# Kernel tuning notes

Measured on AMD Instinct MI355X. Metric: run time of the kernel, lower is better.

The kernel has to match this reference:

```python
import jax, jax.numpy as jnp
import numpy as np

NUM_GROUPS = 32
EPS = 1e-6


def group_norm(x, gamma, beta):
    # x: [b, c, h, w]
    b, c, h, w = x.shape
    g = NUM_GROUPS
    xg = x.reshape(b, g, c // g, h, w)
    mean = xg.mean(axis=(2, 3, 4), keepdims=True)
    var = xg.var(axis=(2, 3, 4), keepdims=True)
    xn = ((xg - mean) * jax.lax.rsqrt(var + EPS)).reshape(b, c, h, w)
    return xn * gamma[None, :, None, None] + beta[None, :, None, None]


def conv1x1(x, w, b):
    # x: [b, c, h, w], w: [out_c, in_c], b: [out_c]
    return jnp.einsum('bchw,oc->bohw', x, w) + b[None, :, None, None]


def setup_inputs() -> dict:
    key = jax.random.key(0)
    ks = jax.random.split(key, 11)
    B, C, H, W = 4, 512, 64, 64
    s = 1.0 / np.sqrt(C)
    inp = {
        'x': jax.random.normal(ks[0], (B, C, H, W), dtype=jnp.float32),
        'gn_gamma': jnp.ones((C,), dtype=jnp.float32),
        'gn_beta': jnp.zeros((C,), dtype=jnp.float32),
        'wq': jax.random.normal(ks[1], (C, C), dtype=jnp.float32) * s,
        'bq': jax.random.normal(ks[2], (C,), dtype=jnp.float32) * 0.01,
        'wk': jax.random.normal(ks[3], (C, C), dtype=jnp.float32) * s,
        'bk': jax.random.normal(ks[4], (C,), dtype=jnp.float32) * 0.01,
        'wv': jax.random.normal(ks[5], (C, C), dtype=jnp.float32) * s,
        'bv': jax.random.normal(ks[6], (C,), dtype=jnp.float32) * 0.01,
        'wo': jax.random.normal(ks[7], (C, C), dtype=jnp.float32) * s,
        'bo': jax.random.normal(ks[8], (C,), dtype=jnp.float32) * 0.01,
    }
    return inp


def reference(x, gn_gamma, gn_beta, wq, bq, wk, bk, wv, bv, wo, bo):
    b, c, h, w = x.shape
    h_ = group_norm(x, gn_gamma, gn_beta)
    q = conv1x1(h_, wq, bq).reshape(b, c, h * w)  # [b, c, n]
    k = conv1x1(h_, wk, bk).reshape(b, c, h * w)
    v = conv1x1(h_, wv, bv).reshape(b, c, h * w)
    scale = jnp.asarray(c, x.dtype) ** -0.5
    # attn[b, i, j] = softmax_j(q_i . k_j * scale)
    attn = jax.nn.softmax(jnp.einsum('bci,bcj->bij', q, k) * scale, axis=-1)
    # A[b, c, i] = sum_j attn[b, i, j] * v[b, c, j]
    A = jnp.einsum('bij,bcj->bci', attn, v).reshape(b, c, h, w)
    A = conv1x1(A, wo, bo)
    # NOTE: the original module multiplies (not adds) the input by the attention output
    return x * A
```

## Files before the change

kernel.cpp:

```cpp
#include <hip/hip_runtime.h>
#include <hip/hip_bf16.h>
#include <stdint.h>

typedef __bf16 bf16x8 __attribute__((ext_vector_type(8)));
typedef __bf16 bf16x4 __attribute__((ext_vector_type(4)));
typedef float f32x4 __attribute__((ext_vector_type(4)));

__device__ __forceinline__ void gload_lds16(const __bf16* g, __bf16* l) {
  __builtin_amdgcn_global_load_lds(
      (const __attribute__((address_space(1))) void*)g,
      (__attribute__((address_space(3))) void*)l, 16, 0, 0);
}

__global__ __launch_bounds__(256) void cvt4_kernel(const float* __restrict__ s0,
                                                   const float* __restrict__ s1,
                                                   const float* __restrict__ s2,
                                                   const float* __restrict__ s3,
                                                   __bf16* __restrict__ dst) {
  int i = blockIdx.x * 256 + threadIdx.x;
  const float* srcs[4] = {s0, s1, s2, s3};
  int m = i >> 18;
  dst[i] = (__bf16)srcs[m][i & 262143];
}

__global__ __launch_bounds__(256) void biascat_kernel(const float* __restrict__ bq,
                                                      const float* __restrict__ bk,
                                                      float* __restrict__ bqk) {
  int i = blockIdx.x * 256 + threadIdx.x;
  bqk[i] = (i < 512) ? bq[i] : bk[i - 512];
}

__global__ __launch_bounds__(256) void gn1a_kernel(const float* __restrict__ x,
                                                   __bf16* __restrict__ xbf,
                                                   float2* __restrict__ part) {
  const int tid = threadIdx.x;
  const size_t base4 = ((size_t)blockIdx.x * 8192) >> 2;
  const float4* x4 = (const float4*)x;
  bf16x4* o4 = (bf16x4*)xbf;

  float s1 = 0.f, s2 = 0.f;
#pragma unroll
  for (int j = 0; j < 8; ++j) {
    float4 t = x4[base4 + tid + j * 256];
    s1 += t.x + t.y + t.z + t.w;
    s2 += t.x * t.x + t.y * t.y + t.z * t.z + t.w * t.w;
    bf16x4 o;
    o[0] = (__bf16)t.x; o[1] = (__bf16)t.y; o[2] = (__bf16)t.z; o[3] = (__bf16)t.w;
    o4[base4 + tid + j * 256] = o;
  }
#pragma unroll
  for (int off = 32; off; off >>= 1) {
    s1 += __shfl_xor(s1, off);
    s2 += __shfl_xor(s2, off);
  }
  __shared__ float r1[4], r2[4];
  if ((tid & 63) == 0) { r1[tid >> 6] = s1; r2[tid >> 6] = s2; }
  __syncthreads();
  if (tid == 0)
    part[blockIdx.x] = float2{r1[0] + r1[1] + r1[2] + r1[3],
                              r2[0] + r2[1] + r2[2] + r2[3]};
}

__global__ __launch_bounds__(512) void gn1b_kernel(const float2* __restrict__ part,
                                                   const float* __restrict__ gamma,
                                                   const float* __restrict__ beta,
                                                   float2* __restrict__ gmbt) {
  const int b = blockIdx.x;
  const int t = threadIdx.x;
  __shared__ float sm[32], si[32];
  if (t < 32) {
    float s1 = 0.f, s2 = 0.f;
#pragma unroll
    for (int j = 0; j < 8; ++j) {
      float2 p = part[(b * 32 + t) * 8 + j];
      s1 += p.x; s2 += p.y;
    }
    const float mean = s1 * (1.f / 65536.f);
    const float var = s2 * (1.f / 65536.f) - mean * mean;
    sm[t] = mean;
    si[t] = rsqrtf(var + 1e-6f);
  }
  __syncthreads();
  const int g = t >> 4;
  const float gm = gamma[t] * si[g];
  gmbt[b * 512 + t] = float2{gm, beta[t] - sm[g] * gm};
}

__global__ __launch_bounds__(256) void gn2_kernel(const __bf16* __restrict__ xbf,
                                                  const float2* __restrict__ gmbt,
                                                  __bf16* __restrict__ hnT) {
  const int b = blockIdx.z;
  const int c0 = blockIdx.y * 64;
  const int n0 = blockIdx.x * 64;
  const int t = threadIdx.x;
  __shared__ __bf16 tile[64][72];

  {
    const int row = t >> 2;
    const int col = (t & 3) * 16;
    const __bf16* src = xbf + ((size_t)(b * 512 + c0 + row)) * 4096 + n0 + col;
    bf16x8 u0 = *(const bf16x8*)src;
    bf16x8 u1 = *(const bf16x8*)(src + 8);
    *(bf16x8*)&tile[row][col] = u0;
    *(bf16x8*)&tile[row][col + 8] = u1;
  }
  __syncthreads();
  {
    const int nrow = t >> 2;
    const int cc = (t & 3) * 16;
    bf16x8 o0, o1;
#pragma unroll
    for (int j = 0; j < 16; ++j) {
      const int c = c0 + cc + j;
      float2 s = gmbt[b * 512 + c];
      float val = (float)tile[cc + j][nrow] * s.x + s.y;
      if (j < 8) o0[j] = (__bf16)val; else o1[j - 8] = (__bf16)val;
    }
    __bf16* dst = hnT + ((size_t)b * 4096 + n0 + nrow) * 512 + c0 + cc;
    *(bf16x8*)dst = o0;
    *(bf16x8*)(dst + 8) = o1;
  }
}

__global__ __launch_bounds__(256) void rowsum_inv_kernel(const __bf16* __restrict__ P,
                                                         float* __restrict__ inv) {
  const int r = blockIdx.x * 4 + (threadIdx.x >> 6);
  const int lane = threadIdx.x & 63;
  const bf16x8* rp = (const bf16x8*)(P + (size_t)r * 4096);
  float s = 0.f;
#pragma unroll
  for (int j = 0; j < 8; ++j) {
    bf16x8 v = rp[lane + j * 64];
#pragma unroll
    for (int e = 0; e < 8; ++e) s += (float)v[e];
  }
#pragma unroll
  for (int off = 32; off; off >>= 1) s += __shfl_xor(s, off);
  if (lane == 0) inv[r] = 1.0f / s;
}

template <int BIAS, int EEXP, int RSCALE, int KC>
__global__ __launch_bounds__(256) void gemm4w_kernel(
    const __bf16* __restrict__ A, int lda, long long sA,
    const __bf16* __restrict__ Bm, int ldb, long long sB,
    __bf16* __restrict__ Out, int ldo, long long sO,
    const float* __restrict__ bias, const float* __restrict__ rowinv,
    float scale) {
  constexpr int SLOT = 4096;
  constexpr int BST = 72;
  __shared__ __bf16 sm[8 * SLOT];
  __bf16* smB = sm + 4 * SLOT;

  const int gx = gridDim.x, gxy = gx * gridDim.y;
  const int nwg = gxy * gridDim.z;
  int bid = blockIdx.x + gx * blockIdx.y + gxy * blockIdx.z;
  bid = (bid & 7) * (nwg >> 3) + (bid >> 3);
  const int bz = bid / gxy;
  const int rem = bid - bz * gxy;
  const int by = rem / gx, bx = rem - by * gx;
  const int tm0 = by * 128, tn0 = bx * 128;

  const int t = threadIdx.x;
  const int lane = t & 63, wid = t >> 6;
  const int wr = wid >> 1, wc = wid & 1;

  const __bf16* Az = A + (size_t)bz * sA;
  const __bf16* Bz = Bm + (size_t)bz * sB;

  const int scol = ((t & 3) * 8) ^ (((t >> 3) & 3) * 8);
  const __bf16* gA0 = Az + (size_t)(tm0 + (t >> 2)) * lda + scol;
  const __bf16* gA1 = gA0 + (size_t)64 * lda;
  const __bf16* gB0 = Bz + (size_t)(tn0 + (t >> 2)) * ldb + scol;
  const __bf16* gB1 = gB0 + (size_t)64 * ldb;
  __bf16* dA = sm + t * 8;
  __bf16* dB = smB + t * 8;

  auto stage = [&](int ks) {
    const int sl = ks & 3;
    gload_lds16(gA0 + (size_t)ks * 32, dA + sl * SLOT);
    gload_lds16(gA1 + (size_t)ks * 32, dA + sl * SLOT + 2048);
    gload_lds16(gB0 + (size_t)ks * 32, dB + sl * SLOT);
    gload_lds16(gB1 + (size_t)ks * 32, dB + sl * SLOT + 2048);
  };

  const int lr = lane & 15;
  const int kb = ((lane >> 4) * 16) ^ ((lr & 6) << 3);
  const __bf16* rdA = sm + (((wr * 64 + lr) * 64 + kb) >> 1);
  const __bf16* rdB = smB + (((wc * 64 + lr) * 64 + kb) >> 1);

  f32x4 acc[4][4];
#pragma unroll
  for (int i = 0; i < 4; ++i)
#pragma unroll
    for (int j = 0; j < 4; ++j) acc[i][j] = f32x4{0.f, 0.f, 0.f, 0.f};
  bf16x8 av[4], bv[4];

  auto rdfr = [&](int sl) {
#pragma unroll
    for (int m = 0; m < 4; ++m) av[m] = *(const bf16x8*)(rdA + sl * SLOT + m * 512);
#pragma unroll
    for (int n = 0; n < 4; ++n) bv[n] = *(const bf16x8*)(rdB + sl * SLOT + n * 512);
  };
  auto mma16 = [&] {
    __builtin_amdgcn_s_barrier();
    __builtin_amdgcn_s_setprio(1);
#pragma unroll
    for (int m = 0; m < 4; ++m)
#pragma unroll
      for (int n = 0; n < 4; ++n)
        acc[m][n] = __builtin_amdgcn_mfma_f32_16x16x32_bf16(av[m], bv[n], acc[m][n], 0, 0, 0);
    __builtin_amdgcn_s_setprio(0);
  };

  constexpr int TOT = KC / 32;

  stage(0); stage(1); stage(2);
  asm volatile("s_waitcnt vmcnt(8)" ::: "memory");
  __builtin_amdgcn_s_barrier();

#pragma unroll 1
  for (int s = 0; s < TOT - 3; ++s) {
    rdfr(s & 3);
    stage(s + 3);
    mma16();
    asm volatile("s_waitcnt vmcnt(8)" ::: "memory");
    __builtin_amdgcn_s_barrier();
  }
  rdfr((TOT - 3) & 3); mma16();
  asm volatile("s_waitcnt vmcnt(4)" ::: "memory");
  __builtin_amdgcn_s_barrier();
  rdfr((TOT - 2) & 3); mma16();
  asm volatile("s_waitcnt vmcnt(0)" ::: "memory");
  __builtin_amdgcn_s_barrier();
  rdfr((TOT - 1) & 3); mma16();
  __builtin_amdgcn_s_barrier();

  __bf16* bnc = sm + wid * 16 * BST;
  const int q4 = (lane >> 4) * 4;
  const int row0 = tm0 + wr * 64;
  const int wn = tn0 + wc * 64;
  float bcol[4];
#pragma unroll
  for (int n = 0; n < 4; ++n) bcol[n] = BIAS ? bias[wn + n * 16 + lr] : 0.f;
#pragma unroll
  for (int m = 0; m < 4; ++m) {
    float ri[4];
    if constexpr (RSCALE) {
#pragma unroll
      for (int r = 0; r < 4; ++r)
        ri[r] = rowinv[(size_t)bz * 4096 + row0 + m * 16 + q4 + r];
    }
#pragma unroll
    for (int n = 0; n < 4; ++n)
#pragma unroll
      for (int r = 0; r < 4; ++r) {
        float val = acc[m][n][r] * scale + bcol[n];
        if constexpr (EEXP) val = exp2f(val * 1.44269504f);
        if constexpr (RSCALE) val *= ri[r];
        bnc[(q4 + r) * BST + n * 16 + lr] = (__bf16)val;
      }
    const int rr = lane >> 3, c8 = (lane & 7) * 8;
    bf16x8 v0 = *(const bf16x8*)&bnc[rr * BST + c8];
    bf16x8 v1 = *(const bf16x8*)&bnc[(rr + 8) * BST + c8];
    __bf16* op = Out + (size_t)bz * sO +
                 (size_t)(row0 + m * 16 + rr) * ldo + wn + c8;
    *(bf16x8*)op = v0;
    *(bf16x8*)(op + (size_t)8 * ldo) = v1;
  }
}

template <int EPI, int BIAS>
__global__ __launch_bounds__(256) void gemm_lds_kernel(
    const __bf16* __restrict__ A, int lda, long long sA,
    const __bf16* __restrict__ Bm, int ldb, long long sB,
    void* __restrict__ Out, int ldo, long long sO,
    const float* __restrict__ bias, const __bf16* __restrict__ xmul,
    long long sX, float scale, int K) {
  __shared__ __bf16 sTa[2][128 * 32];
  __shared__ __bf16 sTb[2][128 * 32];

  const int gx = gridDim.x, gxy = gx * gridDim.y;
  const int nwg = gxy * gridDim.z;
  int bid = blockIdx.x + gx * blockIdx.y + gxy * blockIdx.z;
  if ((nwg & 7) == 0) bid = (bid & 7) * (nwg >> 3) + (bid >> 3);
  const int bz = bid / gxy;
  const int rem = bid - bz * gxy;
  const int by = rem / gx;
  const int bx = rem - by * gx;

  const int tid = threadIdx.x;
  const int lane = tid & 63;
  const int wid = tid >> 6;
  const int wr = wid >> 1, wc = wid & 1;
  const int tm0 = by * 128, tn0 = bx * 128;
  const int lr = lane & 15, lk = (lane >> 4) * 8;

  const int ch0 = wid * 2;
  const int srow = lane >> 2;
  const int scol = (lane & 3) * 8;
  const __bf16* gA0 = A + (size_t)bz * sA + (size_t)(tm0 + ch0 * 16 + srow) * lda + scol;
  const __bf16* gB0 = Bm + (size_t)bz * sB + (size_t)(tn0 + ch0 * 16 + srow) * ldb + scol;
  const size_t stepA = (size_t)16 * lda, stepB = (size_t)16 * ldb;

  f32x4 acc[4][4];
#pragma unroll
  for (int i = 0; i < 4; ++i)
#pragma unroll
    for (int j = 0; j < 4; ++j) acc[i][j] = f32x4{0.f, 0.f, 0.f, 0.f};

  const int T = K >> 5;
  gload_lds16(gA0, &sTa[0][ch0 * 512]);
  gload_lds16(gA0 + stepA, &sTa[0][ch0 * 512 + 512]);
  gload_lds16(gB0, &sTb[0][ch0 * 512]);
  gload_lds16(gB0 + stepB, &sTb[0][ch0 * 512 + 512]);

  for (int tt = 0; tt < T; ++tt) {
    __syncthreads();
    const int cur = tt & 1;
    if (tt + 1 < T) {
      const __bf16* a = gA0 + (size_t)(tt + 1) * 32;
      const __bf16* b = gB0 + (size_t)(tt + 1) * 32;
      gload_lds16(a, &sTa[cur ^ 1][ch0 * 512]);
      gload_lds16(a + stepA, &sTa[cur ^ 1][ch0 * 512 + 512]);
      gload_lds16(b, &sTb[cur ^ 1][ch0 * 512]);
      gload_lds16(b + stepB, &sTb[cur ^ 1][ch0 * 512 + 512]);
    }
    const __bf16* fa = &sTa[cur][(wr * 64 + lr) * 32 + lk];
    const __bf16* fb = &sTb[cur][(wc * 64 + lr) * 32 + lk];
    bf16x8 a[4], b[4];
#pragma unroll
    for (int i = 0; i < 4; ++i) a[i] = *(const bf16x8*)(fa + i * 512);
#pragma unroll
    for (int j = 0; j < 4; ++j) b[j] = *(const bf16x8*)(fb + j * 512);
#pragma unroll
    for (int i = 0; i < 4; ++i)
#pragma unroll
      for (int j = 0; j < 4; ++j)
        acc[i][j] = __builtin_amdgcn_mfma_f32_16x16x32_bf16(a[i], b[j], acc[i][j], 0, 0, 0);
  }

  const int wm = tm0 + wr * 64, wn = tn0 + wc * 64;
#pragma unroll
  for (int i = 0; i < 4; ++i) {
#pragma unroll
    for (int r = 0; r < 4; ++r) {
      const int row = wm + i * 16 + (lane >> 4) * 4 + r;
#pragma unroll
      for (int j = 0; j < 4; ++j) {
        const int col = wn + j * 16 + lr;
        float val = acc[i][j][r] * scale;
        if (BIAS == 1) val += bias[col];
        if (BIAS == 2) val += bias[row];
        const size_t off = (size_t)bz * sO + (size_t)row * ldo + col;
        if (EPI == 0) {
          ((__bf16*)Out)[off] = (__bf16)val;
        } else if (EPI == 1) {
          ((float*)Out)[off] = val;
        } else {
          ((float*)Out)[off] = (float)xmul[(size_t)bz * sX + (size_t)row * ldo + col] * val;
        }
      }
    }
  }
}

extern "C" void kernel_launch(void* const* d_in, const int* in_sizes, int n_in,
                              void* d_out, int out_size, void* d_ws, size_t ws_size,
                              hipStream_t stream) {
  const int C = 512, N = 4096;
  const float* x = (const float*)d_in[0];
  const float* gng = (const float*)d_in[1];
  const float* gnb = (const float*)d_in[2];
  const float* wq = (const float*)d_in[3];
  const float* bq = (const float*)d_in[4];
  const float* wk = (const float*)d_in[5];
  const float* bk = (const float*)d_in[6];
  const float* wv = (const float*)d_in[7];
  const float* bv = (const float*)d_in[8];
  const float* wo = (const float*)d_in[9];
  const float* bo = (const float*)d_in[10];

  char* ws = (char*)d_ws;
  const size_t MB = 1ull << 20;
  const long long NC = (long long)N * C;
  const long long NN = (long long)N * N;
  const long long NQK = (long long)N * 1024;
  const bool batched = ws_size >= 194 * MB + 32768;

  __bf16 *S, *qkT, *a2T, *v, *xbf, *wqB;
  char* misc;
  if (batched) {
    S   = (__bf16*)(ws);
    qkT = (__bf16*)(ws + 128 * MB);
    a2T = qkT;
    v   = (__bf16*)(ws + 160 * MB);
    xbf = (__bf16*)(ws + 176 * MB);
    wqB = (__bf16*)(ws + 192 * MB);
    misc = ws + 194 * MB;
  } else {
    S   = (__bf16*)(ws);
    qkT = (__bf16*)(ws + 32 * MB);
    a2T = (__bf16*)(ws + 64 * MB);
    v   = (__bf16*)(ws + 80 * MB);
    xbf = (__bf16*)(ws + 96 * MB);
    wqB = (__bf16*)(ws + 112 * MB);
    misc = ws + 114 * MB;
  }
  __bf16* hnT = (__bf16*)ws;
  __bf16* wvB = wqB + 2 * 262144;
  __bf16* woB = wvB + 262144;
  float* bqk   = (float*)misc;
  float2* gmbt = (float2*)(misc + 4096);
  float2* part = (float2*)(misc + 20480);
  float* rowInv = (float*)d_out;

  const float scl = 0.044194173824159216f;

  cvt4_kernel<<<4096, 256, 0, stream>>>(wq, wk, wv, wo, wqB);
  biascat_kernel<<<4, 256, 0, stream>>>(bq, bk, bqk);
  gn1a_kernel<<<1024, 256, 0, stream>>>(x, xbf, part);
  gn1b_kernel<<<4, 512, 0, stream>>>(part, gng, gnb, gmbt);
  gn2_kernel<<<dim3(64, 8, 4), 256, 0, stream>>>(xbf, gmbt, hnT);

  gemm4w_kernel<1, 0, 0, 512><<<dim3(8, 32, 4), 256, 0, stream>>>(
      hnT, C, NC, wqB, C, 0, qkT, 1024, NQK, bqk, nullptr, 1.f);
  gemm_lds_kernel<0, 2><<<dim3(32, 4, 4), 256, 0, stream>>>(
      wvB, C, 0, hnT, C, NC, v, N, NC, bv, nullptr, 0, 1.f, C);

  if (batched) {
    gemm4w_kernel<0, 1, 0, 512><<<dim3(32, 32, 4), 256, 0, stream>>>(
        qkT, 1024, NQK, qkT + 512, 1024, NQK, S, N, NN, nullptr, nullptr, scl);
    rowsum_inv_kernel<<<4096, 256, 0, stream>>>(S, rowInv);
    gemm4w_kernel<0, 0, 1, 4096><<<dim3(4, 32, 4), 256, 0, stream>>>(
        S, N, NN, v, N, NC, a2T, C, NC, nullptr, rowInv, 1.f);
  } else {
    for (int b = 0; b < 4; ++b) {
      gemm4w_kernel<0, 1, 0, 512><<<dim3(32, 32, 1), 256, 0, stream>>>(
          qkT + (size_t)b * NQK, 1024, 0, qkT + (size_t)b * NQK + 512, 1024, 0,
          S, N, 0, nullptr, nullptr, scl);
      rowsum_inv_kernel<<<1024, 256, 0, stream>>>(S, rowInv);
      gemm4w_kernel<0, 0, 1, 4096><<<dim3(4, 32, 1), 256, 0, stream>>>(
          S, N, 0, v + (size_t)b * NC, N, 0, a2T + (size_t)b * NC, C, 0,
          nullptr, rowInv, 1.f);
    }
  }

  gemm_lds_kernel<2, 2><<<dim3(32, 4, 4), 256, 0, stream>>>(
      woB, C, 0, a2T, C, NC, (float*)d_out, N, NC, bo, xbf, NC, 1.f, C);
}
```

Baseline: 289.1 us.

## Fuse softmax rowsum into PV GEMM, add large-tile QK exp kernel, unify GEMMs

Removes the separate rowsum kernel by computing row sums of the exponentiated scores inside the P·V GEMM, using an extra MFMA against a ones vector, and normalising in the epilogue. Adds a dedicated 512-thread QK^T+exp kernel with 1024x256 tiles that reuses each loaded K tile across four row sub-tiles. Replaces the older double-buffered gemm_lds kernel for the V projection and output projection with the 4-stage gemm4w pipeline. The trade-offs are extra MFMA work, higher register pressure in the large-tile kernel, and a much smaller grid for QK.

New measurement: 264.2 us. -8.6%, faster.

```diff
diff --git a/kernel.cpp b/kernel.cpp
--- a/kernel.cpp
+++ b/kernel.cpp
@@ -122,30 +122,145 @@
   }
 }
 
-__global__ __launch_bounds__(256) void rowsum_inv_kernel(const __bf16* __restrict__ P,
-                                                         float* __restrict__ inv) {
-  const int r = blockIdx.x * 4 + (threadIdx.x >> 6);
-  const int lane = threadIdx.x & 63;
-  const bf16x8* rp = (const bf16x8*)(P + (size_t)r * 4096);
-  float s = 0.f;
-#pragma unroll
-  for (int j = 0; j < 8; ++j) {
-    bf16x8 v = rp[lane + j * 64];
-#pragma unroll
-    for (int e = 0; e < 8; ++e) s += (float)v[e];
-  }
-#pragma unroll
-  for (int off = 32; off; off >>= 1) s += __shfl_xor(s, off);
-  if (lane == 0) inv[r] = 1.0f / s;
-}
-
-template <int BIAS, int EEXP, int RSCALE, int KC>
+__global__ __launch_bounds__(512) void qkexp_kernel(
+    const __bf16* __restrict__ q, const __bf16* __restrict__ k,
+    __bf16* __restrict__ S, long long sQ, long long sS, float scale) {
+  constexpr int BST = 72;
+  __shared__ __bf16 sm[8 * 8192 + 8 * 16 * BST];
+  __bf16* smB = sm + 4 * 8192;
+  __bf16* smE = sm + 8 * 8192;
+
+  const int gx = gridDim.x, gxy = gx * gridDim.y;
+  const int nwg = gxy * gridDim.z;
+  int bid = blockIdx.x + gx * blockIdx.y + gxy * blockIdx.z;
+  bid = (bid & 7) * (nwg >> 3) + (bid >> 3);
+  const int bz = bid / gxy;
+  const int rem = bid - bz * gxy;
+  const int by = rem / gx, bx = rem - by * gx;
+  const int tm0 = by * 1024, tn0 = bx * 256;
+
+  const int t = threadIdx.x;
+  const int lane = t & 63, wid = t >> 6;
+  const int wr = wid >> 2, wc = wid & 3;
+
+  const int scol = ((t & 3) * 8) ^ (((t >> 3) & 3) * 8);
+  const __bf16* gA0 = q + (size_t)bz * sQ + (size_t)(tm0 + (t >> 2)) * 1024 + scol;
+  const __bf16* gA1 = gA0 + (size_t)128 * 1024;
+  const __bf16* gB0 = k + (size_t)bz * sQ + (size_t)(tn0 + (t >> 2)) * 1024 + scol;
+  const __bf16* gB1 = gB0 + (size_t)128 * 1024;
+  __bf16* dA = sm + t * 8;
+  __bf16* dB = smB + t * 8;
+
+  auto stageA = [&](int sig) {
+    const int st_ = sig >> 4, ks = sig & 15, sl = sig & 3;
+    const size_t off = (size_t)(st_ * 256) * 1024 + ks * 32;
+    gload_lds16(gA0 + off, dA + sl * 8192);
+    gload_lds16(gA1 + off, dA + sl * 8192 + 4096);
+  };
+  auto stageB = [&](int sig) {
+    const int ks = sig & 15, sl = sig & 3;
+    gload_lds16(gB0 + ks * 32, dB + sl * 8192);
+    gload_lds16(gB1 + ks * 32, dB + sl * 8192 + 4096);
+  };
+
+  const int lr = lane & 15;
+  const int kb = ((lane >> 4) * 16) ^ ((lr & 6) << 3);
+  const __bf16* rdA = sm + (((wr * 128 + lr) * 64 + kb) >> 1);
+  const __bf16* rdB = smB + (((wc * 64 + lr) * 64 + kb) >> 1);
+
+  f32x4 acc[8][4];
+#pragma unroll
+  for (int m = 0; m < 8; ++m)
+#pragma unroll
+    for (int n = 0; n < 4; ++n) acc[m][n] = f32x4{0.f, 0.f, 0.f, 0.f};
+  bf16x8 av[8];
+
+  auto rdAfr = [&](int sl) {
+#pragma unroll
+    for (int m = 0; m < 8; ++m)
+      av[m] = *(const bf16x8*)(rdA + sl * 8192 + m * 512);
+  };
+  auto mmaPh = [&](int sl, int nh) {
+    bf16x8 bv[2];
+#pragma unroll
+    for (int j = 0; j < 2; ++j)
+      bv[j] = *(const bf16x8*)(rdB + sl * 8192 + (nh * 2 + j) * 512);
+    __builtin_amdgcn_s_barrier();
+    __builtin_amdgcn_s_setprio(1);
+#pragma unroll
+    for (int m = 0; m < 8; ++m)
+#pragma unroll
+      for (int j = 0; j < 2; ++j)
+        acc[m][nh * 2 + j] = __builtin_amdgcn_mfma_f32_16x16x32_bf16(
+            av[m], bv[j], acc[m][nh * 2 + j], 0, 0, 0);
+    __builtin_amdgcn_s_setprio(0);
+    __builtin_amdgcn_s_barrier();
+  };
+
+  __bf16* bnc = smE + wid * 16 * BST;
+  const int q4 = (lane >> 4) * 4;
+  auto epilogue = [&](int st) {
+    const int row0 = tm0 + st * 256 + wr * 128;
+    const int wn = tn0 + wc * 64;
+#pragma unroll
+    for (int m = 0; m < 8; ++m) {
+#pragma unroll
+      for (int n = 0; n < 4; ++n)
+#pragma unroll
+        for (int r = 0; r < 4; ++r) {
+          float val = acc[m][n][r] * scale;
+          val = exp2f(val * 1.44269504f);
+          bnc[(q4 + r) * BST + n * 16 + lr] = (__bf16)val;
+        }
+      const int rr = lane >> 3, c8 = (lane & 7) * 8;
+      bf16x8 v0 = *(const bf16x8*)&bnc[rr * BST + c8];
+      bf16x8 v1 = *(const bf16x8*)&bnc[(rr + 8) * BST + c8];
+      __bf16* op = S + (size_t)bz * sS +
+                   (size_t)(row0 + m * 16 + rr) * 4096 + wn + c8;
+      *(bf16x8*)op = v0;
+      *(bf16x8*)(op + (size_t)8 * 4096) = v1;
+    }
+  };
+
+  stageA(0); stageB(0); stageA(1); stageB(1); stageA(2); stageB(2);
+  asm volatile("s_waitcnt vmcnt(8)" ::: "memory");
+  __builtin_amdgcn_s_barrier();
+
+#pragma unroll 1
+  for (int s = 0; s < 64; ++s) {
+    const int sl = s & 3;
+    rdAfr(sl);
+    if (s + 3 < 64) stageA(s + 3);
+    mmaPh(sl, 0);
+    if (s + 3 < 64) stageB(s + 3);
+    if (s >= 61) {
+      if (s == 61) asm volatile("s_waitcnt vmcnt(4)" ::: "memory");
+      else if (s == 62) asm volatile("s_waitcnt vmcnt(0)" ::: "memory");
+    } else if ((s & 15) <= 1 && s > 15) {
+      asm volatile("s_waitcnt vmcnt(24)" ::: "memory");
+    } else {
+      asm volatile("s_waitcnt vmcnt(8)" ::: "memory");
+    }
+    mmaPh(sl, 1);
+    if ((s & 15) == 15) {
+      epilogue(s >> 4);
+      if (s < 63) {
+#pragma unroll
+        for (int m = 0; m < 8; ++m)
+#pragma unroll
+          for (int n = 0; n < 4; ++n) acc[m][n] = f32x4{0.f, 0.f, 0.f, 0.f};
+      }
+    }
+  }
+}
+
+template <int BIASMODE, int RSUM, int EPI, int KC>
 __global__ __launch_bounds__(256) void gemm4w_kernel(
     const __bf16* __restrict__ A, int lda, long long sA,
     const __bf16* __restrict__ Bm, int ldb, long long sB,
-    __bf16* __restrict__ Out, int ldo, long long sO,
-    const float* __restrict__ bias, const float* __restrict__ rowinv,
-    float scale) {
+    void* __restrict__ Out, int ldo, long long sO,
+    const float* __restrict__ bias, const __bf16* __restrict__ xmul,
+    long long sX, float scale) {
   constexpr int SLOT = 4096;
   constexpr int BST = 72;
   __shared__ __bf16 sm[8 * SLOT];
@@ -193,6 +308,13 @@
   for (int i = 0; i < 4; ++i)
 #pragma unroll
     for (int j = 0; j < 4; ++j) acc[i][j] = f32x4{0.f, 0.f, 0.f, 0.f};
+  f32x4 acc1[4];
+#pragma unroll
+  for (int i = 0; i < 4; ++i) acc1[i] = f32x4{0.f, 0.f, 0.f, 0.f};
+  bf16x8 onesf;
+#pragma unroll
+  for (int e = 0; e < 8; ++e) onesf[e] = (__bf16)1.0f;
+
   bf16x8 av[4], bv[4];
 
   auto rdfr = [&](int sl) {
@@ -209,6 +331,11 @@
 #pragma unroll
       for (int n = 0; n < 4; ++n)
         acc[m][n] = __builtin_amdgcn_mfma_f32_16x16x32_bf16(av[m], bv[n], acc[m][n], 0, 0, 0);
+    if constexpr (RSUM) {
+#pragma unroll
+      for (int m = 0; m < 4; ++m)
+        acc1[m] = __builtin_amdgcn_mfma_f32_16x16x32_bf16(av[m], onesf, acc1[m], 0, 0, 0);
+    }
     __builtin_amdgcn_s_setprio(0);
   };
 
@@ -235,129 +362,51 @@
   rdfr((TOT - 1) & 3); mma16();
   __builtin_amdgcn_s_barrier();
 
-  __bf16* bnc = sm + wid * 16 * BST;
   const int q4 = (lane >> 4) * 4;
   const int row0 = tm0 + wr * 64;
   const int wn = tn0 + wc * 64;
-  float bcol[4];
-#pragma unroll
-  for (int n = 0; n < 4; ++n) bcol[n] = BIAS ? bias[wn + n * 16 + lr] : 0.f;
-#pragma unroll
-  for (int m = 0; m < 4; ++m) {
-    float ri[4];
-    if constexpr (RSCALE) {
-#pragma unroll
-      for (int r = 0; r < 4; ++r)
-        ri[r] = rowinv[(size_t)bz * 4096 + row0 + m * 16 + q4 + r];
-    }
-#pragma unroll
-    for (int n = 0; n < 4; ++n)
+  if constexpr (EPI == 0) {
+    __bf16* bnc = sm + wid * 16 * BST;
+#pragma unroll
+    for (int m = 0; m < 4; ++m) {
+      float ri[4];
+      if constexpr (RSUM) {
+#pragma unroll
+        for (int r = 0; r < 4; ++r) ri[r] = 1.0f / acc1[m][r];
+      }
+#pragma unroll
+      for (int n = 0; n < 4; ++n)
+#pragma unroll
+        for (int r = 0; r < 4; ++r) {
+          float val = acc[m][n][r] * scale;
+          if constexpr (BIASMODE == 1) val += bias[wn + n * 16 + lr];
+          if constexpr (BIASMODE == 2) val += bias[row0 + m * 16 + q4 + r];
+          if constexpr (RSUM) val *= ri[r];
+          bnc[(q4 + r) * BST + n * 16 + lr] = (__bf16)val;
+        }
+      const int rr = lane >> 3, c8 = (lane & 7) * 8;
+      bf16x8 v0 = *(const bf16x8*)&bnc[rr * BST + c8];
+      bf16x8 v1 = *(const bf16x8*)&bnc[(rr + 8) * BST + c8];
+      __bf16* op = (__bf16*)Out + (size_t)bz * sO +
+                   (size_t)(row0 + m * 16 + rr) * ldo + wn + c8;
+      *(bf16x8*)op = v0;
+      *(bf16x8*)(op + (size_t)8 * ldo) = v1;
+    }
+  } else {
+#pragma unroll
+    for (int m = 0; m < 4; ++m) {
 #pragma unroll
       for (int r = 0; r < 4; ++r) {
-        float val = acc[m][n][r] * scale + bcol[n];
-        if constexpr (EEXP) val = exp2f(val * 1.44269504f);
-        if constexpr (RSCALE) val *= ri[r];
-        bnc[(q4 + r) * BST + n * 16 + lr] = (__bf16)val;
-      }
-    const int rr = lane >> 3, c8 = (lane & 7) * 8;
-    bf16x8 v0 = *(const bf16x8*)&bnc[rr * BST + c8];
-    bf16x8 v1 = *(const bf16x8*)&bnc[(rr + 8) * BST + c8];
-    __bf16* op = Out + (size_t)bz * sO +
-                 (size_t)(row0 + m * 16 + rr) * ldo + wn + c8;
-    *(bf16x8*)op = v0;
-    *(bf16x8*)(op + (size_t)8 * ldo) = v1;
-  }
-}
-
-template <int EPI, int BIAS>
-__global__ __launch_bounds__(256) void gemm_lds_kernel(
-    const __bf16* __restrict__ A, int lda, long long sA,
-    const __bf16* __restrict__ Bm, int ldb, long long sB,
-    void* __restrict__ Out, int ldo, long long sO,
-    const float* __restrict__ bias, const __bf16* __restrict__ xmul,
-    long long sX, float scale, int K) {
-  __shared__ __bf16 sTa[2][128 * 32];
-  __shared__ __bf16 sTb[2][128 * 32];
-
-  const int gx = gridDim.x, gxy = gx * gridDim.y;
-  const int nwg = gxy * gridDim.z;
-  int bid = blockIdx.x + gx * blockIdx.y + gxy * blockIdx.z;
-  if ((nwg & 7) == 0) bid = (bid & 7) * (nwg >> 3) + (bid >> 3);
-  const int bz = bid / gxy;
-  const int rem = bid - bz * gxy;
-  const int by = rem / gx;
-  const int bx = rem - by * gx;
-
-  const int tid = threadIdx.x;
-  const int lane = tid & 63;
-  const int wid = tid >> 6;
-  const int wr = wid >> 1, wc = wid & 1;
-  const int tm0 = by * 128, tn0 = bx * 128;
-  const int lr = lane & 15, lk = (lane >> 4) * 8;
-
-  const int ch0 = wid * 2;
-  const int srow = lane >> 2;
-  const int scol = (lane & 3) * 8;
-  const __bf16* gA0 = A + (size_t)bz * sA + (size_t)(tm0 + ch0 * 16 + srow) * lda + scol;
-  const __bf16* gB0 = Bm + (size_t)bz * sB + (size_t)(tn0 + ch0 * 16 + srow) * ldb + scol;
-  const size_t stepA = (size_t)16 * lda, stepB = (size_t)16 * ldb;
-
-  f32x4 acc[4][4];
-#pragma unroll
-  for (int i = 0; i < 4; ++i)
-#pragma unroll
-    for (int j = 0; j < 4; ++j) acc[i][j] = f32x4{0.f, 0.f, 0.f, 0.f};
-
-  const int T = K >> 5;
-  gload_lds16(gA0, &sTa[0][ch0 * 512]);
-  gload_lds16(gA0 + stepA, &sTa[0][ch0 * 512 + 512]);
-  gload_lds16(gB0, &sTb[0][ch0 * 512]);
-  gload_lds16(gB0 + stepB, &sTb[0][ch0 * 512 + 512]);
-
-  for (int tt = 0; tt < T; ++tt) {
-    __syncthreads();
-    const int cur = tt & 1;
-    if (tt + 1 < T) {
-      const __bf16* a = gA0 + (size_t)(tt + 1) * 32;
-      const __bf16* b = gB0 + (size_t)(tt + 1) * 32;
-      gload_lds16(a, &sTa[cur ^ 1][ch0 * 512]);
-      gload_lds16(a + stepA, &sTa[cur ^ 1][ch0 * 512 + 512]);
-      gload_lds16(b, &sTb[cur ^ 1][ch0 * 512]);
-      gload_lds16(b + stepB, &sTb[cur ^ 1][ch0 * 512 + 512]);
-    }
-    const __bf16* fa = &sTa[cur][(wr * 64 + lr) * 32 + lk];
-    const __bf16* fb = &sTb[cur][(wc * 64 + lr) * 32 + lk];
-    bf16x8 a[4], b[4];
-#pragma unroll
-    for (int i = 0; i < 4; ++i) a[i] = *(const bf16x8*)(fa + i * 512);
-#pragma unroll
-    for (int j = 0; j < 4; ++j) b[j] = *(const bf16x8*)(fb + j * 512);
-#pragma unroll
-    for (int i = 0; i < 4; ++i)
-#pragma unroll
-      for (int j = 0; j < 4; ++j)
-        acc[i][j] = __builtin_amdgcn_mfma_f32_16x16x32_bf16(a[i], b[j], acc[i][j], 0, 0, 0);
-  }
-
-  const int wm = tm0 + wr * 64, wn = tn0 + wc * 64;
-#pragma unroll
-  for (int i = 0; i < 4; ++i) {
-#pragma unroll
-    for (int r = 0; r < 4; ++r) {
-      const int row = wm + i * 16 + (lane >> 4) * 4 + r;
-#pragma unroll
-      for (int j = 0; j < 4; ++j) {
-        const int col = wn + j * 16 + lr;
-        float val = acc[i][j][r] * scale;
-        if (BIAS == 1) val += bias[col];
-        if (BIAS == 2) val += bias[row];
-        const size_t off = (size_t)bz * sO + (size_t)row * ldo + col;
-        if (EPI == 0) {
-          ((__bf16*)Out)[off] = (__bf16)val;
-        } else if (EPI == 1) {
-          ((float*)Out)[off] = val;
-        } else {
-          ((float*)Out)[off] = (float)xmul[(size_t)bz * sX + (size_t)row * ldo + col] * val;
+        const int row = row0 + m * 16 + q4 + r;
+        float brow = (BIASMODE == 2) ? bias[row] : 0.f;
+        const size_t base = (size_t)bz * sO + (size_t)row * ldo;
+#pragma unroll
+        for (int n = 0; n < 4; ++n) {
+          const int col = wn + n * 16 + lr;
+          float val = acc[m][n][r] * scale + brow;
+          if constexpr (BIASMODE == 1) val += bias[col];
+          ((float*)Out)[base + col] =
+              (float)xmul[(size_t)bz * sX + (size_t)row * ldo + col] * val;
         }
       }
     }
@@ -412,7 +461,6 @@
   float* bqk   = (float*)misc;
   float2* gmbt = (float2*)(misc + 4096);
   float2* part = (float2*)(misc + 20480);
-  float* rowInv = (float*)d_out;
 
   const float scl = 0.044194173824159216f;
 
@@ -423,28 +471,25 @@
   gn2_kernel<<<dim3(64, 8, 4), 256, 0, stream>>>(xbf, gmbt, hnT);
 
   gemm4w_kernel<1, 0, 0, 512><<<dim3(8, 32, 4), 256, 0, stream>>>(
-      hnT, C, NC, wqB, C, 0, qkT, 1024, NQK, bqk, nullptr, 1.f);
-  gemm_lds_kernel<0, 2><<<dim3(32, 4, 4), 256, 0, stream>>>(
-      wvB, C, 0, hnT, C, NC, v, N, NC, bv, nullptr, 0, 1.f, C);
+      hnT, C, NC, wqB, C, 0, qkT, 1024, NQK, bqk, nullptr, 0, 1.f);
+  gemm4w_kernel<2, 0, 0, 512><<<dim3(32, 4, 4), 256, 0, stream>>>(
+      wvB, C, 0, hnT, C, NC, v, N, NC, bv, nullptr, 0, 1.f);
 
   if (batched) {
-    gemm4w_kernel<0, 1, 0, 512><<<dim3(32, 32, 4), 256, 0, stream>>>(
-        qkT, 1024, NQK, qkT + 512, 1024, NQK, S, N, NN, nullptr, nullptr, scl);
-    rowsum_inv_kernel<<<4096, 256, 0, stream>>>(S, rowInv);
-    gemm4w_kernel<0, 0, 1, 4096><<<dim3(4, 32, 4), 256, 0, stream>>>(
-        S, N, NN, v, N, NC, a2T, C, NC, nullptr, rowInv, 1.f);
+    qkexp_kernel<<<dim3(16, 4, 4), 512, 0, stream>>>(
+        qkT, qkT + 512, S, NQK, NN, scl);
+    gemm4w_kernel<0, 1, 0, 4096><<<dim3(4, 32, 4), 256, 0, stream>>>(
+        S, N, NN, v, N, NC, a2T, C, NC, nullptr, nullptr, 0, 1.f);
   } else {
     for (int b = 0; b < 4; ++b) {
-      gemm4w_kernel<0, 1, 0, 512><<<dim3(32, 32, 1), 256, 0, stream>>>(
-          qkT + (size_t)b * NQK, 1024, 0, qkT + (size_t)b * NQK + 512, 1024, 0,
-          S, N, 0, nullptr, nullptr, scl);
-      rowsum_inv_kernel<<<1024, 256, 0, stream>>>(S, rowInv);
-      gemm4w_kernel<0, 0, 1, 4096><<<dim3(4, 32, 1), 256, 0, stream>>>(
+      qkexp_kernel<<<dim3(16, 4, 1), 512, 0, stream>>>(
+          qkT + (size_t)b * NQK, qkT + (size_t)b * NQK + 512, S, 0, 0, scl);
+      gemm4w_kernel<0, 1, 0, 4096><<<dim3(4, 32, 1), 256, 0, stream>>>(
           S, N, 0, v + (size_t)b * NC, N, 0, a2T + (size_t)b * NC, C, 0,
-          nullptr, rowInv, 1.f);
-    }
-  }
-
-  gemm_lds_kernel<2, 2><<<dim3(32, 4, 4), 256, 0, stream>>>(
-      woB, C, 0, a2T, C, NC, (float*)d_out, N, NC, bo, xbf, NC, 1.f, C);
-}
+          nullptr, nullptr, 0, 1.f);
+    }
+  }
+
+  gemm4w_kernel<2, 0, 2, 512><<<dim3(32, 4, 4), 256, 0, stream>>>(
+      woB, C, 0, a2T, C, NC, d_out, N, NC, bo, xbf, NC, 1.f);
+}
```
